# Kernel tuning notes

Measured on AMD Instinct MI355X. Metric: run time of the kernel, lower is better.

## Reference

```python
import jax, jax.numpy as jnp
import numpy as np

D_MODEL = 1024
HEADS = 16
D_HEAD = D_MODEL // HEADS


def relative_shift(score):
    # score: [b, h, n, 2n-1] -> [b, h, n, n] via the pad/reshape skew trick
    b, h, n, r = score.shape  # r == 2n - 1
    score = jnp.pad(score, ((0, 0), (0, 0), (0, 0), (1, 0)))  # [b,h,n,2n]
    score = score.reshape(b, h, n * 2 * n)[:, :, n:].reshape(b, h, n, 2 * n - 1)
    return score[..., :n]


def setup_inputs() -> dict:
    key = jax.random.key(0)
    ks = jax.random.split(key, 16)
    b, n, d = 4, 1024, D_MODEL
    s = 1.0 / np.sqrt(d)
    inp = {
        "query": jax.random.normal(ks[0], (b, n, d), jnp.float32),
        "key": jax.random.normal(ks[1], (b, n, d), jnp.float32),
        "value": jax.random.normal(ks[2], (b, n, d), jnp.float32),
        "pos_emb": jax.random.normal(ks[3], (b, 2 * n - 1, d), jnp.float32),
        "Wq": jax.random.normal(ks[4], (d, d), jnp.float32) * s,
        "bq": jnp.zeros((d,), jnp.float32),
        "Wk": jax.random.normal(ks[5], (d, d), jnp.float32) * s,
        "bk": jnp.zeros((d,), jnp.float32),
        "Wv": jax.random.normal(ks[6], (d, d), jnp.float32) * s,
        "bv": jnp.zeros((d,), jnp.float32),
        "Wo": jax.random.normal(ks[7], (d, d), jnp.float32) * s,
        "bo": jnp.zeros((d,), jnp.float32),
        "Wp": jax.random.normal(ks[8], (d, d), jnp.float32) * s,  # pos_proj, no bias
        "u_bias": jax.random.normal(ks[9], (HEADS, D_HEAD), jnp.float32) * 0.05,
        "v_bias": jax.random.normal(ks[10], (HEADS, D_HEAD), jnp.float32) * 0.05,
    }
    return inp


def reference(query, key, value, pos_emb, Wq, bq, Wk, bk, Wv, bv, Wo, bo, Wp, u_bias, v_bias):
    b, n, d = query.shape
    h, dh = HEADS, D_HEAD
    q = (query @ Wq + bq).reshape(b, n, h, dh)            # [b,n,h,dh]
    k = (key @ Wk + bk).reshape(b, n, h, dh)              # [b,n,h,dh]
    v = (value @ Wv + bv).reshape(b, n, h, dh)            # [b,n,h,dh]
    p = (pos_emb @ Wp).reshape(b, 2 * n - 1, h, dh)       # [b,2n-1,h,dh]

    content_score = jnp.einsum('bnhd,bmhd->bhnm', q + u_bias, k)   # [b,h,n,n]
    pos_score = jnp.einsum('bnhd,brhd->bhnr', q + v_bias, p)        # [b,h,n,2n-1]
    pos_score = relative_shift(pos_score)                           # [b,h,n,n]

    score = (content_score + pos_score) / jnp.sqrt(jnp.asarray(d, score_dtype := query.dtype))
    attn = jax.nn.softmax(score, axis=-1)                 # dropout p=0.0 -> identity
    out = jnp.einsum('bhnm,bmhd->bnhd', attn, v).reshape(b, n, d)
    out = out @ Wo + bo
    return out, attn, content_score, pos_score
```

## Files before the change

kernel.cpp:

```cpp
#include <hip/hip_runtime.h>
#include <hip/hip_bf16.h>

typedef __bf16 bf16;
typedef __attribute__((ext_vector_type(8))) __bf16 bf16x8;
typedef __attribute__((ext_vector_type(4))) float f32x4;

#define DEV static __device__ __forceinline__

namespace {

constexpr int B = 4, N = 1024, D = 1024, H = 16, DH = 64;
constexpr int R2 = 2 * N - 1;
constexpr int BH = B * H;
constexpr float SCL = 0.03125f;

DEV bf16 f2b(float x) {
  unsigned u = __builtin_bit_cast(unsigned, x);
  unsigned r = u + 0x7FFFu + ((u >> 16) & 1u);
  unsigned short h = (unsigned short)(r >> 16);
  return __builtin_bit_cast(bf16, h);
}

DEV unsigned cvtpk(float lo, float hi) {
  unsigned r;
  asm("v_cvt_pk_bf16_f32 %0, %1, %2" : "=v"(r) : "v"(lo), "v"(hi));
  return r;
}

DEV bf16x8 cvt8pk(float4 a, float4 b) {
  union { unsigned u[4]; bf16x8 v; } r;
  r.u[0] = cvtpk(a.x, a.y); r.u[1] = cvtpk(a.z, a.w);
  r.u[2] = cvtpk(b.x, b.y); r.u[3] = cvtpk(b.z, b.w);
  return r.v;
}

DEV f32x4 mfma16(bf16x8 a, bf16x8 b, f32x4 c) {
  return __builtin_amdgcn_mfma_f32_16x16x32_bf16(a, b, c, 0, 0, 0);
}

DEV void nt_store4(float4 v, float* p) {
  f32x4 x = {v.x, v.y, v.z, v.w};
  __builtin_nontemporal_store(x, reinterpret_cast<f32x4*>(p));
}

__global__ __launch_bounds__(256) void transpose_cast_w(
    const float* __restrict__ w0, const float* __restrict__ w1,
    const float* __restrict__ w2, const float* __restrict__ w3,
    const float* __restrict__ w4, bf16* __restrict__ t0, bf16* __restrict__ t1,
    bf16* __restrict__ t2, bf16* __restrict__ t3, bf16* __restrict__ t4) {
  const float* src; bf16* dst;
  switch (blockIdx.z) {
    case 0: src = w0; dst = t0; break;
    case 1: src = w1; dst = t1; break;
    case 2: src = w2; dst = t2; break;
    case 3: src = w3; dst = t3; break;
    default: src = w4; dst = t4; break;
  }
  __shared__ float tile[64][65];
  const int k0 = blockIdx.y * 64, n0 = blockIdx.x * 64;
  const int t = threadIdx.x, r = t >> 2, c0 = (t & 3) * 16;
  const float4* sp = reinterpret_cast<const float4*>(src + (size_t)(k0 + r) * D + n0 + c0);
#pragma unroll
  for (int q = 0; q < 4; ++q) {
    float4 v = sp[q];
    tile[r][c0 + q * 4 + 0] = v.x; tile[r][c0 + q * 4 + 1] = v.y;
    tile[r][c0 + q * 4 + 2] = v.z; tile[r][c0 + q * 4 + 3] = v.w;
  }
  __syncthreads();
  union { unsigned u[8]; uint4 q[2]; } pk;
#pragma unroll
  for (int e = 0; e < 8; ++e)
    pk.u[e] = cvtpk(tile[c0 + 2 * e][r], tile[c0 + 2 * e + 1][r]);
  uint4* dp = reinterpret_cast<uint4*>(dst + (size_t)(n0 + r) * D + k0 + c0);
  dp[0] = pk.q[0]; dp[1] = pk.q[1];
}

enum { M_QUV = 0, M_HEAD = 1, M_P = 2, M_OUT = 3 };

template <bool ABF>
DEV void proj_core(char* smem, const void* __restrict__ Av,
                   const bf16* __restrict__ Bt, int M, int mt, int nt, int mode,
                   const float* __restrict__ bias, const float* __restrict__ ubp,
                   const float* __restrict__ vbp, bf16* __restrict__ dst0,
                   bf16* __restrict__ dst1, float* __restrict__ outf) {
  bf16* As = (bf16*)smem;
  bf16* Bs = (bf16*)(smem + 16384);
  float* ep = (float*)smem;
  const int t = threadIdx.x;
  const int m0 = mt * 128, n0 = nt * 128;
  const int lane = t & 63, w = t >> 6;
  const int wi = w >> 1, wj = w & 1;
  const int fr = lane & 15, g = lane >> 4;
  f32x4 acc[4][4] = {};

  int rowc[4], ccc[4], rmc[4];
#pragma unroll
  for (int it = 0; it < 4; ++it) {
    const int chunk = it * 256 + t;
    rowc[it] = chunk >> 3; ccc[it] = chunk & 7;
    int rm = m0 + rowc[it]; rmc[it] = rm < M ? rm : M - 1;
  }
  float4 raf[4][2];
  bf16x8 rab[4];
  bf16x8 rbb[4];
  auto loadstep = [&](int k0) {
#pragma unroll
    for (int it = 0; it < 4; ++it) {
      if (ABF) {
        rab[it] = *reinterpret_cast<const bf16x8*>(
            (const bf16*)Av + (size_t)rmc[it] * D + k0 + ccc[it] * 8);
      } else {
        const float4* ap = reinterpret_cast<const float4*>(
            (const float*)Av + (size_t)rmc[it] * D + k0 + ccc[it] * 8);
        raf[it][0] = ap[0]; raf[it][1] = ap[1];
      }
      rbb[it] = *reinterpret_cast<const bf16x8*>(
          Bt + (size_t)(n0 + rowc[it]) * D + k0 + ccc[it] * 8);
    }
  };

  loadstep(0);
  for (int k0 = 0; k0 < D; k0 += 64) {
#pragma unroll
    for (int it = 0; it < 4; ++it) {
      const int row = rowc[it], cc = ccc[it];
      bf16x8 av;
      if (ABF) av = rab[it]; else av = cvt8pk(raf[it][0], raf[it][1]);
      *reinterpret_cast<bf16x8*>(&As[row * 64 + ((cc ^ (row & 7)) << 3)]) = av;
      *reinterpret_cast<bf16x8*>(&Bs[row * 64 + ((cc ^ (row & 7)) << 3)]) =
          rbb[it];
    }
    __syncthreads();
    if (k0 + 64 < D) loadstep(k0 + 64);
#pragma unroll
    for (int ks = 0; ks < 2; ++ks) {
      bf16x8 fa[4], fb[4];
#pragma unroll
      for (int i = 0; i < 4; ++i) {
        const int row = wi * 64 + i * 16 + fr;
        fa[i] = *reinterpret_cast<const bf16x8*>(
            &As[row * 64 + (((ks * 4 + g) ^ (row & 7)) << 3)]);
      }
#pragma unroll
      for (int j = 0; j < 4; ++j) {
        const int row = wj * 64 + j * 16 + fr;
        fb[j] = *reinterpret_cast<const bf16x8*>(
            &Bs[row * 64 + (((ks * 4 + g) ^ (row & 7)) << 3)]);
      }
#pragma unroll
      for (int i = 0; i < 4; ++i)
#pragma unroll
        for (int j = 0; j < 4; ++j) acc[i][j] = mfma16(fa[i], fb[j], acc[i][j]);
    }
    __syncthreads();
  }
#pragma unroll
  for (int p = 0; p < 2; ++p) {
    __syncthreads();
    if (wi == p) {
#pragma unroll
      for (int i = 0; i < 4; ++i)
#pragma unroll
        for (int j = 0; j < 4; ++j)
#pragma unroll
          for (int q = 0; q < 4; ++q)
            ep[(i * 16 + g * 4 + q) * 132 + wj * 64 + j * 16 + fr] =
                acc[i][j][q];
    }
    __syncthreads();
    const int lr = t >> 2, cl = (t & 3) * 32;
    const int m = m0 + p * 64 + lr;
    if (m < M) {
      float v[32];
#pragma unroll
      for (int kk = 0; kk < 8; ++kk) {
        const float4 f =
            *reinterpret_cast<const float4*>(&ep[lr * 132 + cl + kk * 4]);
        v[kk * 4 + 0] = f.x; v[kk * 4 + 1] = f.y;
        v[kk * 4 + 2] = f.z; v[kk * 4 + 3] = f.w;
      }
      const int cg0 = n0 + cl;
      if (mode == M_OUT) {
        float* op = outf + (size_t)m * D + cg0;
#pragma unroll
        for (int kk = 0; kk < 8; ++kk) {
          float4 f = {v[kk * 4] + bias[cg0 + kk * 4],
                      v[kk * 4 + 1] + bias[cg0 + kk * 4 + 1],
                      v[kk * 4 + 2] + bias[cg0 + kk * 4 + 2],
                      v[kk * 4 + 3] + bias[cg0 + kk * 4 + 3]};
          nt_store4(f, op + kk * 4);
        }
      } else if (mode == M_P) {
        const int b_ = m / R2, r_ = m - b_ * R2;
        const int h_ = cg0 >> 6, dh0 = cg0 & 63;
        bf16* dp = dst0 + (((size_t)(b_ * H + h_)) * R2 + r_) * DH + dh0;
        unsigned pk[16];
#pragma unroll
        for (int e = 0; e < 16; ++e) pk[e] = cvtpk(v[2 * e], v[2 * e + 1]);
#pragma unroll
        for (int kk = 0; kk < 4; ++kk)
          reinterpret_cast<uint4*>(dp)[kk] =
              *reinterpret_cast<const uint4*>(&pk[kk * 4]);
      } else {
        const int b_ = m >> 10, ii = m & (N - 1);
        const int h_ = cg0 >> 6, dh0 = cg0 & 63;
        const size_t o = (((size_t)(b_ * H + h_)) * N + ii) * DH + dh0;
        if (mode == M_QUV) {
          unsigned pku[16], pkv[16];
#pragma unroll
          for (int e = 0; e < 16; ++e) {
            const float b0 = bias[cg0 + 2 * e], b1 = bias[cg0 + 2 * e + 1];
            pku[e] = cvtpk(v[2 * e] + b0 + ubp[cg0 + 2 * e],
                           v[2 * e + 1] + b1 + ubp[cg0 + 2 * e + 1]);
            pkv[e] = cvtpk(v[2 * e] + b0 + vbp[cg0 + 2 * e],
                           v[2 * e + 1] + b1 + vbp[cg0 + 2 * e + 1]);
          }
#pragma unroll
          for (int kk = 0; kk < 4; ++kk) {
            reinterpret_cast<uint4*>(dst0 + o)[kk] =
                *reinterpret_cast<const uint4*>(&pku[kk * 4]);
            reinterpret_cast<uint4*>(dst1 + o)[kk] =
                *reinterpret_cast<const uint4*>(&pkv[kk * 4]);
          }
        } else {
          unsigned pk[16];
#pragma unroll
          for (int e = 0; e < 16; ++e)
            pk[e] = cvtpk(v[2 * e] + bias[cg0 + 2 * e],
                          v[2 * e + 1] + bias[cg0 + 2 * e + 1]);
#pragma unroll
          for (int kk = 0; kk < 4; ++kk)
            reinterpret_cast<uint4*>(dst0 + o)[kk] =
                *reinterpret_cast<const uint4*>(&pk[kk * 4]);
        }
      }
    }
  }
}

__global__ __launch_bounds__(256, 2) void proj_qkvp(
    const float* __restrict__ query, const float* __restrict__ key,
    const float* __restrict__ value, const float* __restrict__ pos_emb,
    const bf16* __restrict__ Wqt, const bf16* __restrict__ Wkt,
    const bf16* __restrict__ Wvt, const bf16* __restrict__ Wpt,
    const float* __restrict__ bq, const float* __restrict__ bk,
    const float* __restrict__ bv, const float* __restrict__ ub,
    const float* __restrict__ vbp, bf16* __restrict__ Qu,
    bf16* __restrict__ Qv, bf16* __restrict__ Kb, bf16* __restrict__ Vb,
    bf16* __restrict__ Pb) {
  __shared__ __align__(16) char smem[34048];
  const int z = blockIdx.z, x = blockIdx.x, y = blockIdx.y;
  if (z < 3 && y >= 32) return;
  const int nt = y & 7;
  const int mt = x * (z == 3 ? 8 : 4) + (y >> 3);
  switch (z) {
    case 0:
      proj_core<false>(smem, query, Wqt, B * N, mt, nt, M_QUV, bq, ub, vbp, Qu,
                       Qv, nullptr);
      break;
    case 1:
      proj_core<false>(smem, key, Wkt, B * N, mt, nt, M_HEAD, bk, nullptr,
                       nullptr, Kb, nullptr, nullptr);
      break;
    case 2:
      proj_core<false>(smem, value, Wvt, B * N, mt, nt, M_HEAD, bv, nullptr,
                       nullptr, Vb, nullptr, nullptr);
      break;
    default:
      proj_core<false>(smem, pos_emb, Wpt, B * R2, mt, nt, M_P, nullptr,
                       nullptr, nullptr, Pb, nullptr, nullptr);
      break;
  }
}

__global__ __launch_bounds__(256, 2) void proj_out(const bf16* __restrict__ OA,
                                                   const bf16* __restrict__ Wot,
                                                   const float* __restrict__ bo,
                                                   float* __restrict__ outF) {
  __shared__ __align__(16) char smem[34048];
  const int nt = blockIdx.y & 7;
  const int mt = blockIdx.x * 4 + (blockIdx.y >> 3);
  proj_core<true>(smem, OA, Wot, B * N, mt, nt, M_OUT, bo, nullptr, nullptr,
                  nullptr, nullptr, outF);
}

__global__ __launch_bounds__(256) void transpose_v(const bf16* __restrict__ V,
                                                   bf16* __restrict__ Vt) {
  __shared__ bf16 tile[64][72];
  const int bh = blockIdx.y, k0 = blockIdx.x * 64;
  const int t = threadIdx.x, r = t >> 2, c0 = (t & 3) * 16;
  const bf16x8* sp =
      reinterpret_cast<const bf16x8*>(V + ((size_t)bh * N + k0 + r) * DH + c0);
  *reinterpret_cast<bf16x8*>(&tile[r][c0]) = sp[0];
  *reinterpret_cast<bf16x8*>(&tile[r][c0 + 8]) = sp[1];
  __syncthreads();
  union { bf16 h[16]; uint4 u[2]; } pk;
#pragma unroll
  for (int e = 0; e < 16; ++e) pk.h[e] = tile[c0 + e][r];
  uint4* dp = reinterpret_cast<uint4*>(Vt + ((size_t)bh * DH + r) * N + k0 + c0);
  dp[0] = pk.u[0]; dp[1] = pk.u[1];
}

constexpr int RB = 16;

DEV int SIDX(int r, int c) {
  return r * 1024 + (((c >> 2) ^ (r & 7)) << 2) + (c & 3);
}

__global__ __launch_bounds__(512, 4) void fused_attn(
    const bf16* __restrict__ Qu, const bf16* __restrict__ Qv,
    const bf16* __restrict__ Kb, const bf16* __restrict__ Pb,
    const bf16* __restrict__ Vt, float* __restrict__ cont,
    float* __restrict__ posS, float* __restrict__ attn,
    bf16* __restrict__ OA) {
  __shared__ float sc[RB * 1024];
  __shared__ float red[1024];
  const int bid0 = blockIdx.y * 64 + blockIdx.x;
  const int bid = (bid0 & 7) * 512 + (bid0 >> 3);
  const int bh = bid >> 6, i0 = (bid & 63) * RB;
  const int t = threadIdx.x, lane = t & 63, w = t >> 6;
  const int fr = lane & 15, g = lane >> 4, kg = g * 8;

  {
    const bf16* Qub = Qu + ((size_t)bh * N + i0) * DH;
    const bf16* Kbh = Kb + (size_t)bh * N * DH;
    const bf16x8 fa0 = *reinterpret_cast<const bf16x8*>(Qub + (size_t)fr * DH + kg);
    const bf16x8 fa1 = *reinterpret_cast<const bf16x8*>(Qub + (size_t)fr * DH + 32 + kg);
#pragma unroll
    for (int tt = 0; tt < 8; ++tt) {
      const int ct = (w * 8 + tt) * 16;
      const bf16x8 fb0 =
          *reinterpret_cast<const bf16x8*>(Kbh + (size_t)(ct + fr) * DH + kg);
      const bf16x8 fb1 =
          *reinterpret_cast<const bf16x8*>(Kbh + (size_t)(ct + fr) * DH + 32 + kg);
      f32x4 acc = {};
      acc = mfma16(fa0, fb0, acc);
      acc = mfma16(fa1, fb1, acc);
      const int c = ct + fr;
#pragma unroll
      for (int q = 0; q < 4; ++q) sc[SIDX(g * 4 + q, c)] = acc[q];
    }
  }
  __syncthreads();

  float4 xc[2][4];
  {
    float* contb = cont + ((size_t)bh * N + i0) * N;
#pragma unroll
    for (int rr2 = 0; rr2 < 2; ++rr2) {
      const int r = w * 2 + rr2;
#pragma unroll
      for (int k = 0; k < 4; ++k) {
        const int ch = (k * 64 + lane) ^ (r & 7);
        xc[rr2][k] = *reinterpret_cast<const float4*>(&sc[r * 1024 + ch * 4]);
      }
#pragma unroll
      for (int k = 0; k < 4; ++k)
        nt_store4(xc[rr2][k], contb + (size_t)r * N + (k * 64 + lane) * 4);
    }
  }
  __syncthreads();

  {
    const bf16* Qvb = Qv + ((size_t)bh * N + i0) * DH;
    const bf16* Pbh = Pb + (size_t)bh * R2 * DH;
    const bf16x8 fa0 = *reinterpret_cast<const bf16x8*>(Qvb + (size_t)fr * DH + kg);
    const bf16x8 fa1 = *reinterpret_cast<const bf16x8*>(Qvb + (size_t)fr * DH + 32 + kg);
    const int Rlo = (N - RB) - i0;
    for (int tt = w; tt < 65; tt += 8) {
      const int rr = Rlo + tt * 16 + fr;
      const int rc = rr < R2 ? rr : R2 - 1;
      const bf16x8 fb0 =
          *reinterpret_cast<const bf16x8*>(Pbh + (size_t)rc * DH + kg);
      const bf16x8 fb1 =
          *reinterpret_cast<const bf16x8*>(Pbh + (size_t)rc * DH + 32 + kg);
      f32x4 acc = {};
      acc = mfma16(fa0, fb0, acc);
      acc = mfma16(fa1, fb1, acc);
#pragma unroll
      for (int q = 0; q < 4; ++q) {
        const int r = g * 4 + q;
        const int jj = rr - (N - 1) + i0 + r;
        if (rr < R2 && jj >= 0 && jj < N) sc[SIDX(r, jj)] = acc[q];
      }
    }
  }
  __syncthreads();

  {
    float* posb = posS + ((size_t)bh * N + i0) * N;
    float* attnb = attn + ((size_t)bh * N + i0) * N;
#pragma unroll
    for (int rr2 = 0; rr2 < 2; ++rr2) {
      const int r = w * 2 + rr2;
      float4 xp[4], x[4];
      int ch[4];
#pragma unroll
      for (int k = 0; k < 4; ++k) {
        ch[k] = (k * 64 + lane) ^ (r & 7);
        xp[k] = *reinterpret_cast<const float4*>(&sc[r * 1024 + ch[k] * 4]);
      }
      float mx = -1e30f;
#pragma unroll
      for (int k = 0; k < 4; ++k) {
        nt_store4(xp[k], posb + (size_t)r * N + (k * 64 + lane) * 4);
        x[k].x = xc[rr2][k].x + xp[k].x; x[k].y = xc[rr2][k].y + xp[k].y;
        x[k].z = xc[rr2][k].z + xp[k].z; x[k].w = xc[rr2][k].w + xp[k].w;
        mx = fmaxf(mx, fmaxf(fmaxf(x[k].x, x[k].y), fmaxf(x[k].z, x[k].w)));
      }
#pragma unroll
      for (int o = 32; o; o >>= 1) mx = fmaxf(mx, __shfl_xor(mx, o));
      float sum = 0.f;
#pragma unroll
      for (int k = 0; k < 4; ++k) {
        x[k].x = __expf((x[k].x - mx) * SCL);
        x[k].y = __expf((x[k].y - mx) * SCL);
        x[k].z = __expf((x[k].z - mx) * SCL);
        x[k].w = __expf((x[k].w - mx) * SCL);
        sum += x[k].x + x[k].y + x[k].z + x[k].w;
      }
#pragma unroll
      for (int o = 32; o; o >>= 1) sum += __shfl_xor(sum, o);
      const float inv = 1.0f / sum;
#pragma unroll
      for (int k = 0; k < 4; ++k) {
        float4 y = {x[k].x * inv, x[k].y * inv, x[k].z * inv, x[k].w * inv};
        nt_store4(y, attnb + (size_t)r * N + (k * 64 + lane) * 4);
        *reinterpret_cast<float4*>(&sc[r * 1024 + ch[k] * 4]) = y;
      }
    }
  }
  __syncthreads();

  {
    const bf16* Vbh = Vt + (size_t)bh * DH * N;
    const int wi = w >> 2, wj = w & 3;
    f32x4 acc = {};
    for (int kt = wi * 16; kt < wi * 16 + 16; ++kt) {
      const int p0 = (kt * 8 + g * 2) ^ (fr & 7);
      const float4 a0 = *reinterpret_cast<const float4*>(&sc[fr * 1024 + p0 * 4]);
      const float4 a1 =
          *reinterpret_cast<const float4*>(&sc[fr * 1024 + (p0 ^ 1) * 4]);
      const bf16x8 fb = *reinterpret_cast<const bf16x8*>(
          Vbh + (size_t)(wj * 16 + fr) * N + kt * 32 + kg);
      acc = mfma16(cvt8pk(a0, a1), fb, acc);
    }
    if (wi == 1) *reinterpret_cast<f32x4*>(&red[(wj * 64 + lane) * 4]) = acc;
    __syncthreads();
    if (wi == 0) {
      const f32x4 o = *reinterpret_cast<const f32x4*>(&red[(wj * 64 + lane) * 4]);
      const int b_ = bh >> 4, h_ = bh & 15;
#pragma unroll
      for (int q = 0; q < 4; ++q) {
        const int row = i0 + g * 4 + q;
        const int dh = wj * 16 + fr;
        OA[((size_t)b_ * N + row) * D + h_ * DH + dh] = f2b(acc[q] + o[q]);
      }
    }
  }
}

}

extern "C" void kernel_launch(void* const* d_in, const int* in_sizes, int n_in,
                              void* d_out, int out_size, void* d_ws,
                              size_t ws_size, hipStream_t stream) {
  (void)in_sizes; (void)n_in; (void)out_size; (void)ws_size;
  const float* query = (const float*)d_in[0];
  const float* key = (const float*)d_in[1];
  const float* value = (const float*)d_in[2];
  const float* pos_emb = (const float*)d_in[3];
  const float* Wq = (const float*)d_in[4];
  const float* bq = (const float*)d_in[5];
  const float* Wk = (const float*)d_in[6];
  const float* bk = (const float*)d_in[7];
  const float* Wv = (const float*)d_in[8];
  const float* bv = (const float*)d_in[9];
  const float* Wo = (const float*)d_in[10];
  const float* bo = (const float*)d_in[11];
  const float* Wp = (const float*)d_in[12];
  const float* ub = (const float*)d_in[13];
  const float* vb = (const float*)d_in[14];

  float* outF = (float*)d_out;
  float* attn = outF + (size_t)B * N * D;
  float* cont = attn + (size_t)BH * N * N;
  float* posS = cont + (size_t)BH * N * N;

  char* wsp = (char*)d_ws;
  auto alloc = [&](size_t elems) {
    bf16* p = (bf16*)wsp;
    wsp += elems * sizeof(bf16);
    return p;
  };
  bf16* Qu = alloc((size_t)BH * N * DH);
  bf16* Qv = alloc((size_t)BH * N * DH);
  bf16* Kb = alloc((size_t)BH * N * DH);
  bf16* Vb = alloc((size_t)BH * N * DH);
  bf16* Vt = alloc((size_t)BH * DH * N);
  bf16* Pb = alloc((size_t)BH * R2 * DH);
  bf16* OA = alloc((size_t)B * N * D);
  bf16* Wqt = alloc((size_t)D * D);
  bf16* Wkt = alloc((size_t)D * D);
  bf16* Wvt = alloc((size_t)D * D);
  bf16* Wpt = alloc((size_t)D * D);
  bf16* Wot = alloc((size_t)D * D);

  dim3 blk(256);
  transpose_cast_w<<<dim3(16, 16, 5), blk, 0, stream>>>(Wq, Wk, Wv, Wp, Wo, Wqt,
                                                        Wkt, Wvt, Wpt, Wot);
  proj_qkvp<<<dim3(8, 64, 4), blk, 0, stream>>>(query, key, value, pos_emb,
                                                Wqt, Wkt, Wvt, Wpt, bq, bk, bv,
                                                ub, vb, Qu, Qv, Kb, Vb, Pb);
  transpose_v<<<dim3(16, 64), blk, 0, stream>>>(Vb, Vt);
  fused_attn<<<dim3(64, 64), dim3(512), 0, stream>>>(Qu, Qv, Kb, Pb, Vt, cont,
                                                     posS, attn, OA);
  proj_out<<<dim3(8, 32), blk, 0, stream>>>(OA, Wot, bo, outF);
}
```

Measured before the change: 348.3 us.

## Use LDS-only barriers, reshape projection grid, and overlap content stores with pos MFMA

```diff
diff --git a/kernel.cpp b/kernel.cpp
--- a/kernel.cpp
+++ b/kernel.cpp
@@ -41,6 +41,13 @@
 DEV void nt_store4(float4 v, float* p) {
   f32x4 x = {v.x, v.y, v.z, v.w};
   __builtin_nontemporal_store(x, reinterpret_cast<f32x4*>(p));
+}
+
+DEV void block_sync_lds() {
+  __builtin_amdgcn_sched_barrier(0);
+  asm volatile("s_waitcnt lgkmcnt(0)" ::: "memory");
+  __builtin_amdgcn_s_barrier();
+  __builtin_amdgcn_sched_barrier(0);
 }
 
 __global__ __launch_bounds__(256) void transpose_cast_w(
@@ -130,7 +137,7 @@
       *reinterpret_cast<bf16x8*>(&Bs[row * 64 + ((cc ^ (row & 7)) << 3)]) =
           rbb[it];
     }
-    __syncthreads();
+    block_sync_lds();
     if (k0 + 64 < D) loadstep(k0 + 64);
 #pragma unroll
     for (int ks = 0; ks < 2; ++ks) {
@@ -152,11 +159,11 @@
 #pragma unroll
         for (int j = 0; j < 4; ++j) acc[i][j] = mfma16(fa[i], fb[j], acc[i][j]);
     }
-    __syncthreads();
+    block_sync_lds();
   }
 #pragma unroll
   for (int p = 0; p < 2; ++p) {
-    __syncthreads();
+    block_sync_lds();
     if (wi == p) {
 #pragma unroll
       for (int i = 0; i < 4; ++i)
@@ -167,7 +174,7 @@
             ep[(i * 16 + g * 4 + q) * 132 + wj * 64 + j * 16 + fr] =
                 acc[i][j][q];
     }
-    __syncthreads();
+    block_sync_lds();
     const int lr = t >> 2, cl = (t & 3) * 32;
     const int m = m0 + p * 64 + lr;
     if (m < M) {
@@ -250,9 +257,8 @@
     bf16* __restrict__ Pb) {
   __shared__ __align__(16) char smem[34048];
   const int z = blockIdx.z, x = blockIdx.x, y = blockIdx.y;
-  if (z < 3 && y >= 32) return;
   const int nt = y & 7;
-  const int mt = x * (z == 3 ? 8 : 4) + (y >> 3);
+  const int mt = x * 4 + (y >> 3);
   switch (z) {
     case 0:
       proj_core<false>(smem, query, Wqt, B * N, mt, nt, M_QUV, bq, ub, vbp, Qu,
@@ -266,8 +272,12 @@
       proj_core<false>(smem, value, Wvt, B * N, mt, nt, M_HEAD, bv, nullptr,
                        nullptr, Vb, nullptr, nullptr);
       break;
+    case 3:
+      proj_core<false>(smem, pos_emb, Wpt, B * R2, mt, nt, M_P, nullptr,
+                       nullptr, nullptr, Pb, nullptr, nullptr);
+      break;
     default:
-      proj_core<false>(smem, pos_emb, Wpt, B * R2, mt, nt, M_P, nullptr,
+      proj_core<false>(smem, pos_emb, Wpt, B * R2, 32 + mt, nt, M_P, nullptr,
                        nullptr, nullptr, Pb, nullptr, nullptr);
       break;
   }
@@ -341,27 +351,29 @@
       for (int q = 0; q < 4; ++q) sc[SIDX(g * 4 + q, c)] = acc[q];
     }
   }
-  __syncthreads();
+  block_sync_lds();
 
   float4 xc[2][4];
+#pragma unroll
+  for (int rr2 = 0; rr2 < 2; ++rr2) {
+    const int r = w * 2 + rr2;
+#pragma unroll
+    for (int k = 0; k < 4; ++k) {
+      const int ch = (k * 64 + lane) ^ (r & 7);
+      xc[rr2][k] = *reinterpret_cast<const float4*>(&sc[r * 1024 + ch * 4]);
+    }
+  }
+  block_sync_lds();
+
   {
     float* contb = cont + ((size_t)bh * N + i0) * N;
 #pragma unroll
     for (int rr2 = 0; rr2 < 2; ++rr2) {
       const int r = w * 2 + rr2;
 #pragma unroll
-      for (int k = 0; k < 4; ++k) {
-        const int ch = (k * 64 + lane) ^ (r & 7);
-        xc[rr2][k] = *reinterpret_cast<const float4*>(&sc[r * 1024 + ch * 4]);
-      }
-#pragma unroll
       for (int k = 0; k < 4; ++k)
         nt_store4(xc[rr2][k], contb + (size_t)r * N + (k * 64 + lane) * 4);
     }
-  }
-  __syncthreads();
-
-  {
     const bf16* Qvb = Qv + ((size_t)bh * N + i0) * DH;
     const bf16* Pbh = Pb + (size_t)bh * R2 * DH;
     const bf16x8 fa0 = *reinterpret_cast<const bf16x8*>(Qvb + (size_t)fr * DH + kg);
@@ -385,7 +397,7 @@
       }
     }
   }
-  __syncthreads();
+  block_sync_lds();
 
   {
     float* posb = posS + ((size_t)bh * N + i0) * N;
@@ -430,7 +442,7 @@
       }
     }
   }
-  __syncthreads();
+  block_sync_lds();
 
   {
     const bf16* Vbh = Vt + (size_t)bh * DH * N;
@@ -446,7 +458,7 @@
       acc = mfma16(cvt8pk(a0, a1), fb, acc);
     }
     if (wi == 1) *reinterpret_cast<f32x4*>(&red[(wj * 64 + lane) * 4]) = acc;
-    __syncthreads();
+    block_sync_lds();
     if (wi == 0) {
       const f32x4 o = *reinterpret_cast<const f32x4*>(&red[(wj * 64 + lane) * 4]);
       const int b_ = bh >> 4, h_ = bh & 15;
@@ -509,7 +521,7 @@
   dim3 blk(256);
   transpose_cast_w<<<dim3(16, 16, 5), blk, 0, stream>>>(Wq, Wk, Wv, Wp, Wo, Wqt,
                                                         Wkt, Wvt, Wpt, Wot);
-  proj_qkvp<<<dim3(8, 64, 4), blk, 0, stream>>>(query, key, value, pos_emb,
+  proj_qkvp<<<dim3(8, 32, 5), blk, 0, stream>>>(query, key, value, pos_emb,
                                                 Wqt, Wkt, Wvt, Wpt, bq, bk, bv,
                                                 ub, vb, Qu, Qv, Kb, Vb, Pb);
   transpose_v<<<dim3(16, 64), blk, 0, stream>>>(Vb, Vt);
```

Result: no change. 350.0 us (+0.5%).
